# Optimization experiments

Measured on AMD Instinct MI355X. Metric: run time of the kernel, lower is better.

The kernel has to match this reference:

```python
import jax, jax.numpy as jnp
import numpy as np

N, M, D = 8192, 8192, 64

def setup_inputs() -> dict:
    key = jax.random.key(0)
    kx, ky = jax.random.split(key)
    x = jax.random.normal(kx, (N, D), dtype=jnp.float32)
    y = jax.random.normal(ky, (M, D), dtype=jnp.float32)
    return {"x": x, "y": y}

def reference(x, y):
    T = 1.0
    # Dmat = 2 - euclidean cdist(x, y), computed via the Gram trick.
    sq = (jnp.sum(x * x, axis=1)[:, None]
          + jnp.sum(y * y, axis=1)[None, :]
          - 2.0 * (x @ y.T))
    Dmat = 2.0 - jnp.sqrt(jnp.maximum(sq, 0.0))          # [N, M]
    logprob_rows = jax.nn.log_softmax(Dmat * T, axis=1)   # [N, M]
    logprob_cols = jax.nn.log_softmax(Dmat.T * T, axis=1) # [M, N]
    choice_rows = jnp.argmax(logprob_rows, axis=1)        # [N]
    choice_cols = jnp.argmax(logprob_cols, axis=1)        # [M]
    seq = jnp.arange(M, dtype=choice_cols.dtype)
    mutual = choice_rows[choice_cols] == seq              # [M] bool
    lp_rows = jnp.take_along_axis(logprob_rows, choice_rows[:, None], axis=1)[:, 0]  # [N]
    lp_cols = jnp.take_along_axis(logprob_cols, choice_cols[:, None], axis=1)[:, 0]  # [M]
    # Padded (jit-friendly) form of the boolean compaction: entries where
    # mutual is False are zeroed; mutual mask identifies valid matches.
    log_probs = jnp.where(mutual, lp_rows[choice_cols] + lp_cols, 0.0)  # [M]
    dmatches = jnp.stack([choice_cols, seq], axis=1)      # [M, 2]
    return (log_probs, dmatches, mutual)
```

## Files before the change

kernel.cpp:

```cpp
#include <hip/hip_runtime.h>
#include <stdint.h>

#define NROWS 8192
#define MCOLS 8192
#define DDIM  64

typedef _Float16 half8   __attribute__((ext_vector_type(8)));
typedef float    floatx4 __attribute__((ext_vector_type(4)));

__device__ __forceinline__ unsigned f2key(float f) {
  unsigned u = __float_as_uint(f);
  return (u & 0x80000000u) ? ~u : (u | 0x80000000u);
}
__device__ __forceinline__ float key2f(unsigned k) {
  unsigned u = (k & 0x80000000u) ? (k & 0x7fffffffu) : ~k;
  return __uint_as_float(u);
}

__global__ void convert_kernel(const float* __restrict__ x, const float* __restrict__ y,
                               _Float16* __restrict__ xh, _Float16* __restrict__ xl,
                               _Float16* __restrict__ yh, _Float16* __restrict__ yl,
                               float* __restrict__ xn, float* __restrict__ yn,
                               unsigned long long* __restrict__ rk,
                               unsigned long long* __restrict__ ck,
                               float* __restrict__ rs, float* __restrict__ cs) {
  __shared__ float lnorm[32];
  const int gid = blockIdx.x * 256 + threadIdx.x;
  if (gid < 8192) { rk[gid] = 0ull; rs[gid] = 0.0f; ck[gid] = 0ull; cs[gid] = 0.0f; }
  if (threadIdx.x < 32) lnorm[threadIdx.x] = 0.0f;
  __syncthreads();

  const float* src; _Float16 *dh, *dl; float* nout; int t, rowbase;
  if (gid < 65536) { src = x; dh = xh; dl = xl; nout = xn; t = gid;
                     rowbase = blockIdx.x * 32; }
  else             { src = y; dh = yh; dl = yl; nout = yn; t = gid - 65536;
                     rowbase = (blockIdx.x - 256) * 32; }

  const int lane = t & 63;
  const int c    = (t >> 6) & 1;
  const int p    = t >> 7;
  const int row  = p * 16 + (lane & 15);
  const int k0   = c * 32 + ((lane >> 4) << 3);
  const float* s = src + (size_t)row * DDIM + k0;

  float fb[8];
  *(floatx4*)(&fb[0]) = *(const floatx4*)(s);
  *(floatx4*)(&fb[4]) = *(const floatx4*)(s + 4);

  _Float16 hbuf[8], lbuf[8];
  float s8 = 0.0f;
  #pragma unroll
  for (int j = 0; j < 8; ++j) {
    float f = fb[j];
    _Float16 h = (_Float16)f;
    hbuf[j] = h;
    lbuf[j] = (_Float16)((f - (float)h) * 2048.0f);
    s8 = fmaf(f, f, s8);
  }
  size_t o = (size_t)t * 8;
  *(half8*)(dh + o) = *(half8*)hbuf;
  *(half8*)(dl + o) = *(half8*)lbuf;

  atomicAdd(&lnorm[((p & 1) << 4) | (t & 15)], s8);
  __syncthreads();
  if (threadIdx.x < 32) nout[rowbase + threadIdx.x] = lnorm[threadIdx.x];
}

#define MFMA16(A, B, C) __builtin_amdgcn_mfma_f32_16x16x32_f16((A), (B), (C), 0, 0, 0)

__global__ __launch_bounds__(256, 4) void mfma_tile_kernel(
    const _Float16* __restrict__ xh, const _Float16* __restrict__ xl,
    const _Float16* __restrict__ yh, const _Float16* __restrict__ yl,
    const float* __restrict__ xn, const float* __restrict__ yn,
    unsigned long long* __restrict__ row_key, float* __restrict__ row_sum,
    unsigned long long* __restrict__ col_key, float* __restrict__ col_sum)
{
  __shared__ unsigned long long lkey[256];
  __shared__ float              lsum[256];

  const int wave = threadIdx.x >> 6;
  const int lane = threadIdx.x & 63;
  const int l15  = lane & 15;
  const int g    = lane >> 4;
  const int ap0  = blockIdx.y * 8 + wave * 2;
  const int ro   = ap0 * 16 + g * 4;
  const int colbase = blockIdx.x * 256;

  lkey[threadIdx.x] = 0ull;
  lsum[threadIdx.x] = 0.0f;
  __syncthreads();

  const half8* xh8 = (const half8*)xh;
  const half8* xl8 = (const half8*)xl;
  const half8* yh8 = (const half8*)yh;
  const half8* yl8 = (const half8*)yl;
  const size_t a0 = (size_t)ap0 * 128 + lane;
  half8 Ah[2][2], Al[2][2];
  #pragma unroll
  for (int p = 0; p < 2; ++p) {
    Ah[p][0] = xh8[a0 + p * 128];      Ah[p][1] = xh8[a0 + p * 128 + 64];
    Al[p][0] = xl8[a0 + p * 128];      Al[p][1] = xl8[a0 + p * 128 + 64];
  }

  float xne[8], rsum[8], rmax[8]; int ridx[8];
  #pragma unroll
  for (int s = 0; s < 8; ++s) {
    xne[s]  = xn[ro + ((s >> 2) << 4) + (s & 3)];
    rsum[s] = 0.0f; rmax[s] = -3.4e38f; ridx[s] = 0;
  }

  const size_t bcol0 = (size_t)(blockIdx.x * 16) * 128 + lane;

  half8 b0h0, b0h1, b0l0, b0l1; float y0n;
  half8 b1h0, b1h1, b1l0, b1l1; float y1n;
  b0h0 = yh8[bcol0];      b0h1 = yh8[bcol0 + 64];
  b0l0 = yl8[bcol0];      b0l1 = yl8[bcol0 + 64];
  y0n  = yn[colbase + l15];

#define STEP(JT, BH0, BH1, BL0, BL1, YNC, NH0, NH1, NL0, NL1, NYN)             \
  {                                                                            \
                   \
    const int jn_ = ((JT) + 1) & 15;                                           \
    const size_t bn_ = bcol0 + (size_t)jn_ * 128;                              \
    NH0 = yh8[bn_];      NH1 = yh8[bn_ + 64];                                  \
    NL0 = yl8[bn_];      NL1 = yl8[bn_ + 64];                                  \
    NYN = yn[colbase + jn_ * 16 + l15];                                        \
    const int col_ = colbase + (JT) * 16 + l15;                                \
    float cmax_ = -3.4e38f; int cidx_ = 0; float epan_[2];                     \
    _Pragma("unroll")                                                          \
    for (int p = 0; p < 2; ++p) {                                              \
      floatx4 c1 = {}, c2 = {};                                                \
      c1 = MFMA16(Ah[p][0], BH0, c1);                                          \
      c1 = MFMA16(Ah[p][1], BH1, c1);                                          \
      c2 = MFMA16(Al[p][0], BH0, c2);                                          \
      c2 = MFMA16(Al[p][1], BH1, c2);                                          \
      c2 = MFMA16(Ah[p][0], BL0, c2);                                          \
      c2 = MFMA16(Ah[p][1], BL1, c2);                                          \
      float ee_[4];                                                            \
      _Pragma("unroll")                                                        \
      for (int r = 0; r < 4; ++r) {                                            \
        const int s_ = p * 4 + r;                                              \
        float dot = fmaf(c2[r], (1.0f / 2048.0f), c1[r]);                      \
        float sq  = fmaxf(fmaf(-2.0f, dot, xne[s_] + (YNC)), 0.0f);            \
        float d   = 2.0f - __builtin_amdgcn_sqrtf(sq);                         \
        float e   = __expf(d);                                                 \
        rsum[s_] += e;                                                         \
        if (d > rmax[s_]) ridx[s_] = col_;       \
        rmax[s_] = fmaxf(rmax[s_], d);                                         \
        if (d > cmax_) cidx_ = s_;             \
        cmax_ = fmaxf(cmax_, d);                                               \
        ee_[r] = e;                                                            \
      }                                                                        \
      epan_[p] = (ee_[0] + ee_[1]) + (ee_[2] + ee_[3]);                        \
    }                                                                          \
    float csum_ = epan_[0] + epan_[1];           \
    int crow_ = ro + ((cidx_ >> 2) << 4) + (cidx_ & 3);                        \
    unsigned long long ckey_ =                                                 \
        ((unsigned long long)f2key(cmax_) << 32) |                             \
        (unsigned long long)(unsigned)(~(unsigned)crow_);                      \
    atomicMax(&lkey[(JT) * 16 + l15], ckey_);       \
    atomicAdd(&lsum[(JT) * 16 + l15], csum_);       \
  }

  for (int jt = 0; jt < 16; jt += 2) {
    STEP(jt,     b0h0, b0h1, b0l0, b0l1, y0n, b1h0, b1h1, b1l0, b1l1, y1n);
    STEP(jt + 1, b1h0, b1h1, b1l0, b1l1, y1n, b0h0, b0h1, b0l0, b0l1, y0n);
  }
#undef STEP

  unsigned long long rkk[8];
  #pragma unroll
  for (int s = 0; s < 8; ++s)
    rkk[s] = ((unsigned long long)f2key(rmax[s]) << 32) |
             (unsigned long long)(unsigned)(~(unsigned)ridx[s]);
  #pragma unroll
  for (int off = 1; off < 16; off <<= 1) {
    #pragma unroll
    for (int s = 0; s < 8; ++s) {
      rsum[s] += __shfl_xor(rsum[s], off);
      unsigned long long o = __shfl_xor(rkk[s], off);
      if (o > rkk[s]) rkk[s] = o;
    }
  }
  if (l15 == 0) {
    #pragma unroll
    for (int s = 0; s < 8; ++s) {
      int row = ro + ((s >> 2) << 4) + (s & 3);
      atomicMax(row_key + row, rkk[s]);
      atomicAdd(row_sum + row, rsum[s]);
    }
  }

  __syncthreads();
  {
    int col = colbase + threadIdx.x;
    atomicMax(col_key + col, lkey[threadIdx.x]);
    atomicAdd(col_sum + col, lsum[threadIdx.x]);
  }
}

__global__ void finalize_kernel(const unsigned long long* __restrict__ row_key,
                                const float* __restrict__ row_sum,
                                const unsigned long long* __restrict__ col_key,
                                const float* __restrict__ col_sum,
                                float* __restrict__ out)
{
  int j = blockIdx.x * 256 + threadIdx.x;
  if (j >= MCOLS) return;
  unsigned long long ck = col_key[j];
  int   ci   = (int)(~(unsigned)ck);
  float cmax = key2f((unsigned)(ck >> 32));
  float lp_col = cmax - logf(col_sum[j]);

  unsigned long long rk = row_key[ci];
  int   rj   = (int)(~(unsigned)rk);
  float rmax = key2f((unsigned)(rk >> 32));
  float lp_row = rmax - logf(row_sum[ci]);

  int mut = (rj == j);
  out[j]                 = mut ? (lp_row + lp_col) : 0.0f;
  out[MCOLS + 2 * j + 0] = (float)ci;
  out[MCOLS + 2 * j + 1] = (float)j;
  out[3 * MCOLS + j]     = mut ? 1.0f : 0.0f;
}

extern "C" void kernel_launch(void* const* d_in, const int* in_sizes, int n_in,
                              void* d_out, int out_size, void* d_ws, size_t ws_size,
                              hipStream_t stream) {
  const float* x = (const float*)d_in[0];
  const float* y = (const float*)d_in[1];
  float* out = (float*)d_out;

  char* ws = (char*)d_ws;
  unsigned long long* row_key = (unsigned long long*)(ws);
  unsigned long long* col_key = (unsigned long long*)(ws + 65536);
  float* row_sum = (float*)(ws + 131072);
  float* col_sum = (float*)(ws + 163840);
  float* xn      = (float*)(ws + 196608);
  float* yn      = (float*)(ws + 229376);
  _Float16* xh = (_Float16*)(ws + 262144);
  _Float16* xl = (_Float16*)(ws + 262144 + 1048576);
  _Float16* yh = (_Float16*)(ws + 262144 + 2097152);
  _Float16* yl = (_Float16*)(ws + 262144 + 3145728);

  convert_kernel<<<512, 256, 0, stream>>>(x, y, xh, xl, yh, yl, xn, yn,
                                          row_key, col_key, row_sum, col_sum);
  dim3 grid(MCOLS / 256, NROWS / 128);
  mfma_tile_kernel<<<grid, 256, 0, stream>>>(xh, xl, yh, yl, xn, yn,
                                             row_key, row_sum, col_key, col_sum);
  finalize_kernel<<<32, 256, 0, stream>>>(row_key, row_sum, col_key, col_sum, out);
}
```

Measured before the change: 129.5 us.

## Software-pipeline MFMA tiles against the previous tile's epilogue

The column-tile loop is restructured so each iteration issues the MFMAs for the next tile before running the sqrt/exp/max epilogue of the current tile. B-operand loads are also prefetched two tiles ahead instead of one. The aim is to hide MFMA latency behind the VALU/transcendental work. The extra accumulator and prefetch registers forced launch bounds down from 4 to 3 waves per SIMD, which lowers occupancy.

Result: faster. 123.8 us (-4.4%).

```diff
diff --git a/kernel.cpp b/kernel.cpp
--- a/kernel.cpp
+++ b/kernel.cpp
@@ -68,7 +68,7 @@
 
 #define MFMA16(A, B, C) __builtin_amdgcn_mfma_f32_16x16x32_f16((A), (B), (C), 0, 0, 0)
 
-__global__ __launch_bounds__(256, 4) void mfma_tile_kernel(
+__global__ __launch_bounds__(256, 3) void mfma_tile_kernel(
     const _Float16* __restrict__ xh, const _Float16* __restrict__ xl,
     const _Float16* __restrict__ yh, const _Float16* __restrict__ yl,
     const float* __restrict__ xn, const float* __restrict__ yn,
@@ -113,60 +113,116 @@
 
   half8 b0h0, b0h1, b0l0, b0l1; float y0n;
   half8 b1h0, b1h1, b1l0, b1l1; float y1n;
-  b0h0 = yh8[bcol0];      b0h1 = yh8[bcol0 + 64];
-  b0l0 = yl8[bcol0];      b0l1 = yl8[bcol0 + 64];
+  b0h0 = yh8[bcol0];        b0h1 = yh8[bcol0 + 64];
+  b0l0 = yl8[bcol0];        b0l1 = yl8[bcol0 + 64];
   y0n  = yn[colbase + l15];
-
-#define STEP(JT, BH0, BH1, BL0, BL1, YNC, NH0, NH1, NL0, NL1, NYN)             \
+  b1h0 = yh8[bcol0 + 128];  b1h1 = yh8[bcol0 + 192];
+  b1l0 = yl8[bcol0 + 128];  b1l1 = yl8[bcol0 + 192];
+  y1n  = yn[colbase + 16 + l15];
+
+#define MFMA_TILE(BH0, BH1, BL0, BL1, O1A, O2A, O1B, O2B)                      \
   {                                                                            \
-                   \
-    const int jn_ = ((JT) + 1) & 15;                                           \
-    const size_t bn_ = bcol0 + (size_t)jn_ * 128;                              \
-    NH0 = yh8[bn_];      NH1 = yh8[bn_ + 64];                                  \
-    NL0 = yl8[bn_];      NL1 = yl8[bn_ + 64];                                  \
-    NYN = yn[colbase + jn_ * 16 + l15];                                        \
+    floatx4 c1_ = {}, c2_ = {};                                                \
+    c1_ = MFMA16(Ah[0][0], BH0, c1_);                                          \
+    c1_ = MFMA16(Ah[0][1], BH1, c1_);                                          \
+    c2_ = MFMA16(Al[0][0], BH0, c2_);                                          \
+    c2_ = MFMA16(Al[0][1], BH1, c2_);                                          \
+    c2_ = MFMA16(Ah[0][0], BL0, c2_);                                          \
+    c2_ = MFMA16(Ah[0][1], BL1, c2_);                                          \
+    O1A = c1_; O2A = c2_;                                                      \
+    floatx4 d1_ = {}, d2_ = {};                                                \
+    d1_ = MFMA16(Ah[1][0], BH0, d1_);                                          \
+    d1_ = MFMA16(Ah[1][1], BH1, d1_);                                          \
+    d2_ = MFMA16(Al[1][0], BH0, d2_);                                          \
+    d2_ = MFMA16(Al[1][1], BH1, d2_);                                          \
+    d2_ = MFMA16(Ah[1][0], BL0, d2_);                                          \
+    d2_ = MFMA16(Ah[1][1], BL1, d2_);                                          \
+    O1B = d1_; O2B = d2_;                                                      \
+  }
+
+#define EPILOGUE(JT, C1A, C2A, C1B, C2B, YNC)                                  \
+  {                                                                            \
     const int col_ = colbase + (JT) * 16 + l15;                                \
-    float cmax_ = -3.4e38f; int cidx_ = 0; float epan_[2];                     \
-    _Pragma("unroll")                                                          \
-    for (int p = 0; p < 2; ++p) {                                              \
-      floatx4 c1 = {}, c2 = {};                                                \
-      c1 = MFMA16(Ah[p][0], BH0, c1);                                          \
-      c1 = MFMA16(Ah[p][1], BH1, c1);                                          \
-      c2 = MFMA16(Al[p][0], BH0, c2);                                          \
-      c2 = MFMA16(Al[p][1], BH1, c2);                                          \
-      c2 = MFMA16(Ah[p][0], BL0, c2);                                          \
-      c2 = MFMA16(Ah[p][1], BL1, c2);                                          \
+    float cmax_ = -3.4e38f; int cidx_ = 0;                                     \
+    float epan0_, epan1_;                                                      \
+    {                                                                          \
       float ee_[4];                                                            \
       _Pragma("unroll")                                                        \
       for (int r = 0; r < 4; ++r) {                                            \
-        const int s_ = p * 4 + r;                                              \
-        float dot = fmaf(c2[r], (1.0f / 2048.0f), c1[r]);                      \
+        const int s_ = r;                                                      \
+        float dot = fmaf(C2A[r], (1.0f / 2048.0f), C1A[r]);                    \
         float sq  = fmaxf(fmaf(-2.0f, dot, xne[s_] + (YNC)), 0.0f);            \
         float d   = 2.0f - __builtin_amdgcn_sqrtf(sq);                         \
         float e   = __expf(d);                                                 \
         rsum[s_] += e;                                                         \
         if (d > rmax[s_]) ridx[s_] = col_;       \
         rmax[s_] = fmaxf(rmax[s_], d);                                         \
-        if (d > cmax_) cidx_ = s_;             \
+        if (d > cmax_) cidx_ = s_;               \
         cmax_ = fmaxf(cmax_, d);                                               \
         ee_[r] = e;                                                            \
       }                                                                        \
-      epan_[p] = (ee_[0] + ee_[1]) + (ee_[2] + ee_[3]);                        \
+      epan0_ = (ee_[0] + ee_[1]) + (ee_[2] + ee_[3]);                          \
     }                                                                          \
-    float csum_ = epan_[0] + epan_[1];           \
+    {                                                                          \
+      float ee_[4];                                                            \
+      _Pragma("unroll")                                                        \
+      for (int r = 0; r < 4; ++r) {                                            \
+        const int s_ = 4 + r;                                                  \
+        float dot = fmaf(C2B[r], (1.0f / 2048.0f), C1B[r]);                    \
+        float sq  = fmaxf(fmaf(-2.0f, dot, xne[s_] + (YNC)), 0.0f);            \
+        float d   = 2.0f - __builtin_amdgcn_sqrtf(sq);                         \
+        float e   = __expf(d);                                                 \
+        rsum[s_] += e;                                                         \
+        if (d > rmax[s_]) ridx[s_] = col_;                                     \
+        rmax[s_] = fmaxf(rmax[s_], d);                                         \
+        if (d > cmax_) cidx_ = s_;                                             \
+        cmax_ = fmaxf(cmax_, d);                                               \
+        ee_[r] = e;                                                            \
+      }                                                                        \
+      epan1_ = (ee_[0] + ee_[1]) + (ee_[2] + ee_[3]);                          \
+    }                                                                          \
+    float csum_ = epan0_ + epan1_;                \
     int crow_ = ro + ((cidx_ >> 2) << 4) + (cidx_ & 3);                        \
     unsigned long long ckey_ =                                                 \
         ((unsigned long long)f2key(cmax_) << 32) |                             \
         (unsigned long long)(unsigned)(~(unsigned)crow_);                      \
-    atomicMax(&lkey[(JT) * 16 + l15], ckey_);       \
-    atomicAdd(&lsum[(JT) * 16 + l15], csum_);       \
-  }
-
-  for (int jt = 0; jt < 16; jt += 2) {
-    STEP(jt,     b0h0, b0h1, b0l0, b0l1, y0n, b1h0, b1h1, b1l0, b1l1, y1n);
-    STEP(jt + 1, b1h0, b1h1, b1l0, b1l1, y1n, b0h0, b0h1, b0l0, b0l1, y0n);
-  }
-#undef STEP
+    atomicMax(&lkey[(JT) * 16 + l15], ckey_);                  \
+    atomicAdd(&lsum[(JT) * 16 + l15], csum_);                  \
+  }
+
+  floatx4 Pc1a, Pc2a, Pc1b, Pc2b;
+  floatx4 Qc1a, Qc2a, Qc1b, Qc2b;
+
+  MFMA_TILE(b0h0, b0h1, b0l0, b0l1, Pc1a, Pc2a, Pc1b, Pc2b);
+
+  for (int jt = 0; jt < 14; jt += 2) {
+    {
+      float ycur = y0n;
+      const size_t bn = bcol0 + (size_t)(jt + 2) * 128;
+      b0h0 = yh8[bn];      b0h1 = yh8[bn + 64];
+      b0l0 = yl8[bn];      b0l1 = yl8[bn + 64];
+      y0n  = yn[colbase + (jt + 2) * 16 + l15];
+      MFMA_TILE(b1h0, b1h1, b1l0, b1l1, Qc1a, Qc2a, Qc1b, Qc2b);
+      EPILOGUE(jt, Pc1a, Pc2a, Pc1b, Pc2b, ycur);
+    }
+    {
+      float ycur = y1n;
+      const size_t bn = bcol0 + (size_t)(jt + 3) * 128;
+      b1h0 = yh8[bn];      b1h1 = yh8[bn + 64];
+      b1l0 = yl8[bn];      b1l1 = yl8[bn + 64];
+      y1n  = yn[colbase + (jt + 3) * 16 + l15];
+      MFMA_TILE(b0h0, b0h1, b0l0, b0l1, Pc1a, Pc2a, Pc1b, Pc2b);
+      EPILOGUE(jt + 1, Qc1a, Qc2a, Qc1b, Qc2b, ycur);
+    }
+  }
+  {
+    MFMA_TILE(b1h0, b1h1, b1l0, b1l1, Qc1a, Qc2a, Qc1b, Qc2b);
+    EPILOGUE(14, Pc1a, Pc2a, Pc1b, Pc2b, y0n);
+  }
+  EPILOGUE(15, Qc1a, Qc2a, Qc1b, Qc2b, y1n);
+
+#undef MFMA_TILE
+#undef EPILOGUE
 
   unsigned long long rkk[8];
   #pragma unroll
```
